# Performance work log

Hardware: AMD Instinct MI355X
Metric: run time of the kernel (lower is better)

Reference implementation:

```python
import jax, jax.numpy as jnp
import numpy as np


def setup_inputs() -> dict:
    key = jax.random.key(0)
    k1, k2, k3, k4, k5 = jax.random.split(key, 5)
    B, C, T, U = 4, 256, 4096, 64
    y1 = jax.random.normal(k1, (B, C, T), dtype=jnp.float32)
    y2 = jax.random.normal(k2, (B, C, T), dtype=jnp.float32)
    # module init: uniform(-0.02, 0.02)
    Wq = jax.random.uniform(k3, (C, U), minval=-0.02, maxval=0.02, dtype=jnp.float32)
    Wk = jax.random.uniform(k4, (C, U), minval=-0.02, maxval=0.02, dtype=jnp.float32)
    Wv = jax.random.uniform(k5, (C, U), minval=-0.02, maxval=0.02, dtype=jnp.float32)
    return {"y1": y1, "y2": y2, "Wq": Wq, "Wk": Wk, "Wv": Wv, "attention_width": 256}


def reference(y1, y2, Wq, Wk, Wv, attention_width):
    # y1, y2: [B, C, T] -> projected to [B, T, U]
    q1 = jnp.einsum('bct,cu->btu', y1, Wq)
    k2 = jnp.einsum('bct,cu->btu', y2, Wk)
    v2 = jnp.einsum('bct,cu->btu', y2, Wv)
    d_k = q1.shape[-1]
    # scores e[b, i, j] = q1[b,i,:] . k2[b,j,:] / sqrt(U)
    e = jnp.einsum('biu,bju->bij', q1, k2) / jnp.sqrt(jnp.float32(d_k))
    T = e.shape[-1]
    # banded mask: keep (i, j) where j - w//2 <= i < j - w//2 + w
    lower = jnp.arange(T) - attention_width // 2          # [T] (per column j)
    upper = lower + attention_width                        # [T]
    i = jnp.arange(T)[:, None]                             # [T, 1] (row index)
    mask = (lower <= i) & (i < upper)                      # [T, T]
    e = jnp.where(mask, e, -jnp.inf)
    a = jax.nn.softmax(e, axis=-1)                         # [B, T, T]
    # out = (a @ v2) then permute(0, 2, 1) -> [B, U, T]
    out = jnp.einsum('bij,bju->bui', a, v2)
    return (out, a)
```

## Files before the change

kernel.cpp:

```cpp
#include <hip/hip_runtime.h>

using uint = unsigned int;
typedef unsigned short ushort_t;
typedef float f32x4 __attribute__((ext_vector_type(4)));
typedef short short8 __attribute__((ext_vector_type(8)));

#define B_ 4
#define C_ 256
#define T_ 4096
#define U_ 64

static __device__ __forceinline__ float bflo(uint w) { return __uint_as_float(w << 16); }
static __device__ __forceinline__ float bfhi(uint w) { return __uint_as_float(w & 0xffff0000u); }
static __device__ __forceinline__ uint f2bf(float f) {
    uint x = __float_as_uint(f);
    return (x + 0x7fffu + ((x >> 16) & 1u)) >> 16;
}

__global__ __launch_bounds__(256) void proj_kernel(
    const float* __restrict__ y1, const float* __restrict__ y2,
    const float* __restrict__ Wq, const float* __restrict__ Wk,
    const float* __restrict__ Wv,
    ushort_t* __restrict__ Qb, ushort_t* __restrict__ Kb, ushort_t* __restrict__ Vt)
{
    __shared__ alignas(16) ushort_t wt[2][64][264];

    const int p   = blockIdx.y;
    const int b   = blockIdx.x >> 6;
    const int t0  = (blockIdx.x & 63) << 6;
    const int tid = threadIdx.x;

    {
        const float* W0 = (p == 0) ? Wq : Wk;
#pragma unroll
        for (int k = 0; k < 64; ++k) {
            int idx = tid + 256 * k;
            int c = idx >> 6, u = idx & 63;
            wt[0][u][c] = (ushort_t)f2bf(W0[idx]);
        }
        if (p == 1) {
#pragma unroll
            for (int k = 0; k < 64; ++k) {
                int idx = tid + 256 * k;
                int c = idx >> 6, u = idx & 63;
                wt[1][u][c] = (ushort_t)f2bf(Wv[idx]);
            }
        }
    }
    __syncthreads();

    const int wid = tid >> 6, l = tid & 63;
    const int lm = l & 15, lg = l >> 4;

    const float* ysrc = ((p == 0) ? y1 : y2) + (size_t)b * (C_ * T_);
    const float* yp   = ysrc + (size_t)(8 * lg) * T_ + (t0 + 16 * wid + lm);

    f32x4 acc0[4] = {};
    f32x4 acc1[4] = {};
#pragma unroll
    for (int ks = 0; ks < 8; ++ks) {
        float av[8];
#pragma unroll
        for (int j = 0; j < 8; ++j)
            av[j] = yp[(size_t)(32 * ks + j) * T_];
        short8 af;
#pragma unroll
        for (int j = 0; j < 8; ++j)
            af[j] = (short)f2bf(av[j]);
#pragma unroll
        for (int n = 0; n < 4; ++n) {
            short8 bq = *(const short8*)&wt[0][16 * n + lm][32 * ks + 8 * lg];
            acc0[n] = __builtin_amdgcn_mfma_f32_16x16x32_bf16(af, bq, acc0[n], 0, 0, 0);
            if (p) {
                short8 bv = *(const short8*)&wt[1][16 * n + lm][32 * ks + 8 * lg];
                acc1[n] = __builtin_amdgcn_mfma_f32_16x16x32_bf16(af, bv, acc1[n], 0, 0, 0);
            }
        }
    }

    ushort_t* O0 = p ? Kb : Qb;
#pragma unroll
    for (int n = 0; n < 4; ++n)
#pragma unroll
        for (int r = 0; r < 4; ++r) {
            int t = t0 + 16 * wid + 4 * lg + r;
            int u = 16 * n + lm;
            O0[((size_t)b * T_ + t) * U_ + u] = (ushort_t)f2bf(acc0[n][r]);
            if (p)
                Vt[((size_t)b * U_ + u) * T_ + t] = (ushort_t)f2bf(acc1[n][r]);
        }
}

__global__ __launch_bounds__(512) void attn_kernel(
    const ushort_t* __restrict__ Qb, const ushort_t* __restrict__ Kb,
    const ushort_t* __restrict__ Vt, float* __restrict__ gout)
{
    __shared__ alignas(16) uint     kw[288 * 32];
    __shared__ alignas(16) ushort_t vt[64][296];
    __shared__ alignas(16) ushort_t alds[32][296];
    __shared__ alignas(16) uint     qlds[32][32];
    __shared__ float sums[8][20];

    const int bid = blockIdx.x;
    const int b   = bid >> 7;
    const int i0  = (bid & 127) << 5;
    const int tid = threadIdx.x;

    const int jb2    = max(0, i0 - 127) & ~7;
    const int jend   = min(T_, i0 + 160);
    const int width2 = jend - jb2;
    const int NT     = width2 >> 4;

    for (int idx = tid; idx < 2304; idx += 512) {
        int row = idx >> 3, q = idx & 7;
        int srow = min(jb2 + row, T_ - 1);
        uint4 v = ((const uint4*)(Kb + ((size_t)b * T_ + srow) * U_))[q];
        *(uint4*)(kw + row * 32 + ((4 * q) ^ ((row & 7) << 2))) = v;
    }
    {
        const int u = tid >> 3, c0 = tid & 7;
        const ushort_t* vrow = Vt + ((size_t)b * U_ + u) * T_ + jb2;
#pragma unroll
        for (int k = 0; k < 5; ++k) {
            int c = c0 + 8 * k;
            if (c < 37) {
                short8 v = {};
                if (8 * c < width2)
                    v = *(const short8*)(vrow + 8 * c);
                *(short8*)&vt[u][8 * c] = v;
            }
        }
    }
    if (tid < 256) {
        const int row = tid >> 3, q = tid & 7;
        uint4 v = ((const uint4*)(Qb + ((size_t)b * T_ + i0 + row) * U_))[q];
        *(uint4*)&qlds[row][(4 * q) ^ ((row & 7) << 2)] = v;
    }
    {
        short8 z = {};
        short8* af = (short8*)&alds[0][0];
        for (int idx = tid; idx < 1184; idx += 512)
            af[idx] = z;
    }
    __syncthreads();

    const int w = tid >> 6, l = tid & 63;
    const int lm = l & 15, lg = l >> 4;
    const int qt = w & 1, jt0 = w >> 1;
    const int selq = (lm & 7) << 2;

    const uint* qr = &qlds[16 * qt + lm][0];
    const short8 aq0 = *(const short8*)(qr + ((4 * lg) ^ selq));
    const short8 aq1 = *(const short8*)(qr + ((16 + 4 * lg) ^ selq));

    f32x4 ev[5];
    f32x4 psum = {};
#pragma unroll
    for (int s = 0; s < 5; ++s) ev[s] = (f32x4)(0.f);
#pragma unroll
    for (int s = 0; s < 5; ++s) {
        const int jt = 4 * s + jt0;
        if (jt < NT) {
            const int row = 16 * jt + lm;
            const uint* kr = kw + row * 32;
            short8 bk0 = *(const short8*)(kr + ((4 * lg) ^ selq));
            short8 bk1 = *(const short8*)(kr + ((16 + 4 * lg) ^ selq));
            f32x4 acc = {};
            acc = __builtin_amdgcn_mfma_f32_16x16x32_bf16(aq0, bk0, acc, 0, 0, 0);
            acc = __builtin_amdgcn_mfma_f32_16x16x32_bf16(aq1, bk1, acc, 0, 0, 0);
            const int j = jb2 + row;
#pragma unroll
            for (int r = 0; r < 4; ++r) {
                int i = i0 + 16 * qt + 4 * lg + r;
                bool val = (j >= i - 127) && (j <= i + 128);
                float e = val ? __expf(acc[r] * 0.125f) : 0.f;
                ev[s][r] = e;
                psum[r] += e;
            }
        }
    }
#pragma unroll
    for (int m = 1; m < 16; m <<= 1) {
#pragma unroll
        for (int r = 0; r < 4; ++r)
            psum[r] += __shfl_xor(psum[r], m, 64);
    }
    if (lm == 0)
        *(f32x4*)&sums[w][4 * lg] = psum;
    __syncthreads();

    f32x4 rtot = *(const f32x4*)&sums[qt][4 * lg];
    rtot += *(const f32x4*)&sums[qt + 2][4 * lg];
    rtot += *(const f32x4*)&sums[qt + 4][4 * lg];
    rtot += *(const f32x4*)&sums[qt + 6][4 * lg];
    f32x4 rinv;
#pragma unroll
    for (int r = 0; r < 4; ++r)
        rinv[r] = __builtin_amdgcn_rcpf(rtot[r]);

#pragma unroll
    for (int s = 0; s < 5; ++s) {
        const int jt = 4 * s + jt0;
        if (jt < NT) {
#pragma unroll
            for (int r = 0; r < 4; ++r) {
                float a = ev[s][r] * rinv[r];
                ev[s][r] = a;
                alds[16 * qt + 4 * lg + r][16 * jt + lm] = (ushort_t)f2bf(a);
            }
        }
    }
    __syncthreads();

    float* aout = gout + (size_t)B_ * U_ * T_;

#pragma unroll
    for (int s = 0; s < 5; ++s) {
        const int jt = 4 * s + jt0;
        if (jt < NT) {
            const int j = jb2 + 16 * jt + lm;
#pragma unroll
            for (int r = 0; r < 4; ++r) {
                int i = i0 + 16 * qt + 4 * lg + r;
                if ((j >= i - 127) && (j <= i + 128))
                    __builtin_nontemporal_store(ev[s][r],
                        aout + ((size_t)b * T_ + i) * T_ + j);
            }
        }
    }
    {
        const f32x4 zz = (f32x4)(0.f);
#pragma unroll
        for (int rr = 0; rr < 4; ++rr) {
            const int i   = i0 + 4 * w + rr;
            const int jlo = max(0, i - 127);
            const int jhi = min(T_ - 1, i + 128);
            float* rowp = aout + ((size_t)b * T_ + i) * T_;
            f32x4* row4 = (f32x4*)rowp;
            int nleft4 = jlo >> 2;
            for (int k = l; k < nleft4; k += 64)
                __builtin_nontemporal_store(zz, row4 + k);
            int rem = jlo & 3;
            if (l < rem)
                __builtin_nontemporal_store(0.f, rowp + (jlo & ~3) + l);
            int js = jhi + 1;
            int ah = (4 - (js & 3)) & 3;
            if (l < ah && js + l < T_)
                __builtin_nontemporal_store(0.f, rowp + js + l);
            int js4 = (js + ah) >> 2;
            for (int k = js4 + l; k < T_ / 4; k += 64)
                __builtin_nontemporal_store(zz, row4 + k);
        }
    }

    {
        const int wu = w >> 1, qp = w & 1;
        f32x4 pacc = {};
#pragma unroll
        for (int kc = 0; kc < 9; ++kc) {
            short8 pa = *(const short8*)&vt[16 * wu + lm][8 * lg + 32 * kc];
            short8 pb = *(const short8*)&alds[16 * qp + lm][8 * lg + 32 * kc];
            pacc = __builtin_amdgcn_mfma_f32_16x16x32_bf16(pa, pb, pacc, 0, 0, 0);
        }
#pragma unroll
        for (int r = 0; r < 4; ++r)
            gout[((size_t)b * U_ + 16 * wu + 4 * lg + r) * T_ + i0 + 16 * qp + lm] = pacc[r];
    }
}

extern "C" void kernel_launch(void* const* d_in, const int* in_sizes, int n_in,
                              void* d_out, int out_size, void* d_ws, size_t ws_size,
                              hipStream_t stream)
{
    const float* y1 = (const float*)d_in[0];
    const float* y2 = (const float*)d_in[1];
    const float* Wq = (const float*)d_in[2];
    const float* Wk = (const float*)d_in[3];
    const float* Wv = (const float*)d_in[4];

    ushort_t* Qb = (ushort_t*)d_ws;
    ushort_t* Kb = Qb + (size_t)B_ * T_ * U_;
    ushort_t* Vt = Kb + (size_t)B_ * T_ * U_;

    float* gout = (float*)d_out;

    proj_kernel<<<dim3(B_ * (T_ / 64), 2), 256, 0, stream>>>(y1, y2, Wq, Wk, Wv, Qb, Kb, Vt);
    attn_kernel<<<512, 512, 0, stream>>>(Qb, Kb, Vt, gout);
}
```

Measured before the change: 86.10 us.

## Shrink attention tiles to 16 rows, load K/V directly from global, drop LDS staging

Result: slower. 90.52 us (+5.1%).

```diff
diff --git a/kernel.cpp b/kernel.cpp
--- a/kernel.cpp
+++ b/kernel.cpp
@@ -10,8 +10,6 @@
 #define T_ 4096
 #define U_ 64
 
-static __device__ __forceinline__ float bflo(uint w) { return __uint_as_float(w << 16); }
-static __device__ __forceinline__ float bfhi(uint w) { return __uint_as_float(w & 0xffff0000u); }
 static __device__ __forceinline__ uint f2bf(float f) {
     uint x = __float_as_uint(f);
     return (x + 0x7fffu + ((x >> 16) & 1u)) >> 16;
@@ -91,67 +89,48 @@
         }
 }
 
-__global__ __launch_bounds__(512) void attn_kernel(
+__global__ __launch_bounds__(256, 8) void attn_kernel(
     const ushort_t* __restrict__ Qb, const ushort_t* __restrict__ Kb,
     const ushort_t* __restrict__ Vt, float* __restrict__ gout)
 {
-    __shared__ alignas(16) uint     kw[288 * 32];
-    __shared__ alignas(16) ushort_t vt[64][296];
-    __shared__ alignas(16) ushort_t alds[32][296];
-    __shared__ alignas(16) uint     qlds[32][32];
-    __shared__ float sums[8][20];
+    __shared__ alignas(16) ushort_t alds[16][296];
+    __shared__ float sums[4][20];
 
     const int bid = blockIdx.x;
-    const int b   = bid >> 7;
-    const int i0  = (bid & 127) << 5;
+    const int b   = bid >> 8;
+    const int i0  = (bid & 255) << 4;
     const int tid = threadIdx.x;
+    const int w   = tid >> 6, l = tid & 63;
+    const int lm  = l & 15, lg = l >> 4;
 
     const int jb2    = max(0, i0 - 127) & ~7;
-    const int jend   = min(T_, i0 + 160);
+    const int jend   = min(T_, i0 + 144);
     const int width2 = jend - jb2;
     const int NT     = width2 >> 4;
 
-    for (int idx = tid; idx < 2304; idx += 512) {
-        int row = idx >> 3, q = idx & 7;
-        int srow = min(jb2 + row, T_ - 1);
-        uint4 v = ((const uint4*)(Kb + ((size_t)b * T_ + srow) * U_))[q];
-        *(uint4*)(kw + row * 32 + ((4 * q) ^ ((row & 7) << 2))) = v;
-    }
-    {
-        const int u = tid >> 3, c0 = tid & 7;
-        const ushort_t* vrow = Vt + ((size_t)b * U_ + u) * T_ + jb2;
-#pragma unroll
-        for (int k = 0; k < 5; ++k) {
-            int c = c0 + 8 * k;
-            if (c < 37) {
-                short8 v = {};
-                if (8 * c < width2)
-                    v = *(const short8*)(vrow + 8 * c);
-                *(short8*)&vt[u][8 * c] = v;
-            }
-        }
-    }
-    if (tid < 256) {
-        const int row = tid >> 3, q = tid & 7;
-        uint4 v = ((const uint4*)(Qb + ((size_t)b * T_ + i0 + row) * U_))[q];
-        *(uint4*)&qlds[row][(4 * q) ^ ((row & 7) << 2)] = v;
-    }
+    const ushort_t* qrow = Qb + ((size_t)b * T_ + i0 + lm) * U_ + 8 * lg;
+    const short8 aq0 = *(const short8*)(qrow);
+    const short8 aq1 = *(const short8*)(qrow + 32);
+
+    short8 pa[9];
+    {
+        const ushort_t* vrow = Vt + ((size_t)(b * U_ + 16 * w + lm)) * T_;
+#pragma unroll
+        for (int kc = 0; kc < 9; ++kc) {
+            int jcol = min(jb2 + 32 * kc + 8 * lg, T_ - 8);
+            pa[kc] = *(const short8*)(vrow + jcol);
+        }
+    }
+
     {
         short8 z = {};
         short8* af = (short8*)&alds[0][0];
-        for (int idx = tid; idx < 1184; idx += 512)
-            af[idx] = z;
-    }
-    __syncthreads();
-
-    const int w = tid >> 6, l = tid & 63;
-    const int lm = l & 15, lg = l >> 4;
-    const int qt = w & 1, jt0 = w >> 1;
-    const int selq = (lm & 7) << 2;
-
-    const uint* qr = &qlds[16 * qt + lm][0];
-    const short8 aq0 = *(const short8*)(qr + ((4 * lg) ^ selq));
-    const short8 aq1 = *(const short8*)(qr + ((16 + 4 * lg) ^ selq));
+#pragma unroll
+        for (int k = 0; k < 3; ++k) {
+            int idx = tid + 256 * k;
+            if (idx < 592) af[idx] = z;
+        }
+    }
 
     f32x4 ev[5];
     f32x4 psum = {};
@@ -159,19 +138,18 @@
     for (int s = 0; s < 5; ++s) ev[s] = (f32x4)(0.f);
 #pragma unroll
     for (int s = 0; s < 5; ++s) {
-        const int jt = 4 * s + jt0;
+        const int jt = 4 * s + w;
         if (jt < NT) {
-            const int row = 16 * jt + lm;
-            const uint* kr = kw + row * 32;
-            short8 bk0 = *(const short8*)(kr + ((4 * lg) ^ selq));
-            short8 bk1 = *(const short8*)(kr + ((16 + 4 * lg) ^ selq));
+            const int j = jb2 + 16 * jt + lm;
+            const ushort_t* kp = Kb + ((size_t)b * T_ + j) * U_ + 8 * lg;
+            short8 bk0 = *(const short8*)(kp);
+            short8 bk1 = *(const short8*)(kp + 32);
             f32x4 acc = {};
             acc = __builtin_amdgcn_mfma_f32_16x16x32_bf16(aq0, bk0, acc, 0, 0, 0);
             acc = __builtin_amdgcn_mfma_f32_16x16x32_bf16(aq1, bk1, acc, 0, 0, 0);
-            const int j = jb2 + row;
 #pragma unroll
             for (int r = 0; r < 4; ++r) {
-                int i = i0 + 16 * qt + 4 * lg + r;
+                int i = i0 + 4 * lg + r;
                 bool val = (j >= i - 127) && (j <= i + 128);
                 float e = val ? __expf(acc[r] * 0.125f) : 0.f;
                 ev[s][r] = e;
@@ -189,10 +167,10 @@
         *(f32x4*)&sums[w][4 * lg] = psum;
     __syncthreads();
 
-    f32x4 rtot = *(const f32x4*)&sums[qt][4 * lg];
-    rtot += *(const f32x4*)&sums[qt + 2][4 * lg];
-    rtot += *(const f32x4*)&sums[qt + 4][4 * lg];
-    rtot += *(const f32x4*)&sums[qt + 6][4 * lg];
+    f32x4 rtot = *(const f32x4*)&sums[0][4 * lg];
+    rtot += *(const f32x4*)&sums[1][4 * lg];
+    rtot += *(const f32x4*)&sums[2][4 * lg];
+    rtot += *(const f32x4*)&sums[3][4 * lg];
     f32x4 rinv;
 #pragma unroll
     for (int r = 0; r < 4; ++r)
@@ -200,13 +178,13 @@
 
 #pragma unroll
     for (int s = 0; s < 5; ++s) {
-        const int jt = 4 * s + jt0;
+        const int jt = 4 * s + w;
         if (jt < NT) {
 #pragma unroll
             for (int r = 0; r < 4; ++r) {
                 float a = ev[s][r] * rinv[r];
                 ev[s][r] = a;
-                alds[16 * qt + 4 * lg + r][16 * jt + lm] = (ushort_t)f2bf(a);
+                alds[4 * lg + r][16 * jt + lm] = (ushort_t)f2bf(a);
             }
         }
     }
@@ -216,15 +194,14 @@
 
 #pragma unroll
     for (int s = 0; s < 5; ++s) {
-        const int jt = 4 * s + jt0;
+        const int jt = 4 * s + w;
         if (jt < NT) {
             const int j = jb2 + 16 * jt + lm;
 #pragma unroll
             for (int r = 0; r < 4; ++r) {
-                int i = i0 + 16 * qt + 4 * lg + r;
+                int i = i0 + 4 * lg + r;
                 if ((j >= i - 127) && (j <= i + 128))
-                    __builtin_nontemporal_store(ev[s][r],
-                        aout + ((size_t)b * T_ + i) * T_ + j);
+                    aout[((size_t)b * T_ + i) * T_ + j] = ev[s][r];
             }
         }
     }
@@ -239,32 +216,30 @@
             f32x4* row4 = (f32x4*)rowp;
             int nleft4 = jlo >> 2;
             for (int k = l; k < nleft4; k += 64)
-                __builtin_nontemporal_store(zz, row4 + k);
+                row4[k] = zz;
             int rem = jlo & 3;
             if (l < rem)
-                __builtin_nontemporal_store(0.f, rowp + (jlo & ~3) + l);
+                rowp[(jlo & ~3) + l] = 0.f;
             int js = jhi + 1;
             int ah = (4 - (js & 3)) & 3;
             if (l < ah && js + l < T_)
-                __builtin_nontemporal_store(0.f, rowp + js + l);
+                rowp[js + l] = 0.f;
             int js4 = (js + ah) >> 2;
             for (int k = js4 + l; k < T_ / 4; k += 64)
-                __builtin_nontemporal_store(zz, row4 + k);
-        }
-    }
-
-    {
-        const int wu = w >> 1, qp = w & 1;
+                row4[k] = zz;
+        }
+    }
+
+    {
         f32x4 pacc = {};
 #pragma unroll
         for (int kc = 0; kc < 9; ++kc) {
-            short8 pa = *(const short8*)&vt[16 * wu + lm][8 * lg + 32 * kc];
-            short8 pb = *(const short8*)&alds[16 * qp + lm][8 * lg + 32 * kc];
-            pacc = __builtin_amdgcn_mfma_f32_16x16x32_bf16(pa, pb, pacc, 0, 0, 0);
+            short8 pb = *(const short8*)&alds[lm][32 * kc + 8 * lg];
+            pacc = __builtin_amdgcn_mfma_f32_16x16x32_bf16(pa[kc], pb, pacc, 0, 0, 0);
         }
 #pragma unroll
         for (int r = 0; r < 4; ++r)
-            gout[((size_t)b * U_ + 16 * wu + 4 * lg + r) * T_ + i0 + 16 * qp + lm] = pacc[r];
+            gout[((size_t)(b * U_ + 16 * w + 4 * lg + r)) * T_ + i0 + lm] = pacc[r];
     }
 }
 
@@ -285,5 +260,5 @@
     float* gout = (float*)d_out;
 
     proj_kernel<<<dim3(B_ * (T_ / 64), 2), 256, 0, stream>>>(y1, y2, Wq, Wk, Wv, Qb, Kb, Vt);
-    attn_kernel<<<512, 512, 0, stream>>>(Qb, Kb, Vt, gout);
-}
+    attn_kernel<<<1024, 256, 0, stream>>>(Qb, Kb, Vt, gout);
+}
```
